# Optimization experiments

Measured on AMD Instinct MI355X. Metric: run time of the kernel, lower is better.

## Reference

```python
import jax, jax.numpy as jnp
import numpy as np

TEMP = 0.07
GAMMA1 = 0.8
GAMMA2 = 0.8
TAU = 0.1
BETA = 40.0
NUM_CT = 5
EPS = float(np.finfo(np.float32).eps)


def setup_inputs() -> dict:
    key = jax.random.key(0)
    ks = jax.random.split(key, 12)
    B, D, N, Bc = 8192, 512, 1000000, 4096
    img = jax.random.normal(ks[0], (B, D), jnp.float32)
    txt = jax.random.normal(ks[1], (B, D), jnp.float32)
    # CLIP-style unit-norm features keep sim in [-1,1] so exp() stays stable
    img = img / jnp.linalg.norm(img, axis=1, keepdims=True)
    txt = txt / jnp.linalg.norm(txt, axis=1, keepdims=True)
    image_ids = jax.random.randint(ks[2], (B,), 0, N)
    text_ids = jax.random.randint(ks[3], (B,), 0, N)
    slabel = jax.random.randint(ks[4], (B,), 0, 2)
    img_feas_c = jax.random.normal(ks[5], (Bc, D), jnp.float32)
    img_feas_c = img_feas_c / jnp.linalg.norm(img_feas_c, axis=1, keepdims=True)
    txt_feas_c = jax.random.normal(ks[6], (NUM_CT, D), jnp.float32)
    txt_feas_c = txt_feas_c / jnp.linalg.norm(txt_feas_c, axis=1, keepdims=True)
    labels_c = jax.random.randint(ks[7], (Bc,), 0, NUM_CT)
    last_loss_c = jax.random.uniform(ks[8], (Bc,), jnp.float32) * 2.0
    # persistent moving-average buffers (positive values, as they hold past exp-means)
    s_I = jax.random.uniform(ks[9], (N,), jnp.float32) + 0.5
    s_T = jax.random.uniform(ks[10], (N,), jnp.float32) + 0.5
    u = jnp.zeros((NUM_CT,), jnp.float32)
    return dict(image_features=img, text_features=txt, image_ids=image_ids,
                text_ids=text_ids, slabel=slabel, epoch=1,
                img_feas_c=img_feas_c, txt_feas_c=txt_feas_c, labels_c=labels_c,
                last_loss_c=last_loss_c, s_I=s_I, s_T=s_T, u=u)


def reference(image_features, text_features, image_ids, text_ids, slabel, epoch,
              img_feas_c, txt_feas_c, labels_c, last_loss_c, s_I, s_T, u):
    sg = jax.lax.stop_gradient
    # pairwise similarity GEMM  [B, B]
    sim = jnp.einsum('id,jd->ij', image_features, text_features)
    diag = jnp.diagonal(sim)
    pos = slabel == 1
    neg = ~pos
    pos_image_ids = image_ids[pos]
    pos_text_ids = text_ids[pos]
    # masked pairwise similarity differences: [P, B-P] and [B-P, P]
    image_diffs = (sim - diag[:, None])[pos][:, neg]
    text_diffs = (sim - diag[None, :])[neg][:, pos]
    image_diffs_d = sg(image_diffs / TEMP)
    text_diffs_d = sg(text_diffs / TEMP)
    exp_i = jnp.exp(image_diffs_d)
    exp_t = jnp.exp(text_diffs_d)
    g_I = jnp.mean(exp_i, axis=1, keepdims=True)   # [P, 1]
    g_T = jnp.mean(exp_t, axis=0, keepdims=True)   # [1, P]
    if epoch == 0:
        sI = g_I
        sT = g_T
    else:
        sI = ((1.0 - GAMMA1) * s_I[pos_image_ids] + GAMMA1 * g_I.squeeze()).reshape(g_I.shape)
        sT = ((1.0 - GAMMA1) * s_T[pos_text_ids] + GAMMA1 * g_T.squeeze()).reshape(g_T.shape)
    # persistent buffer scatter updates
    s_I_new = s_I.at[pos_image_ids].set(sI.squeeze())
    s_T_new = s_T.at[pos_text_ids].set(sT.squeeze())
    w_i = exp_i / (sI + EPS)
    w_t = exp_t / (sT + EPS)
    image_loss = jnp.mean(w_i * image_diffs, axis=1)
    text_loss = jnp.mean(w_t * text_diffs, axis=0)
    contrastive_loss = image_loss.mean() + text_loss.mean()
    # per-class CE penalty branch
    logits = (1.0 / TAU) * img_feas_c @ txt_feas_c.T           # [Bc, NUM_CT]
    logp = jax.nn.log_softmax(logits, axis=-1)
    ce = -logp[jnp.arange(logits.shape[0]), labels_c]          # [Bc]
    counts = jax.ops.segment_sum(jnp.ones_like(ce), labels_c, num_segments=NUM_CT)
    present = counts > 0
    safe_counts = jnp.maximum(counts, 1.0)
    mean_by_cls = jax.ops.segment_sum(ce, labels_c, num_segments=NUM_CT) / safe_counts
    mean_by_cls_last = jax.ops.segment_sum(last_loss_c, labels_c, num_segments=NUM_CT) / safe_counts
    cv = mean_by_cls - mean_by_cls_last
    u_sum = jnp.sum(jnp.where(present, u, 0.0))
    u_upd = jnp.where(u_sum == 0.0, sg(cv), (1.0 - GAMMA2) * u + GAMMA2 * sg(cv))
    u_new = jnp.where(present, u_upd, u)
    beta = BETA  # cosine=False
    cl = sg(jnp.maximum(beta * u_new, 0.0)) * mean_by_cls * TAU
    n_present = jnp.sum(present.astype(jnp.float32))
    constraint_mean = jnp.sum(jnp.where(present, cl, 0.0)) / n_present
    loss = contrastive_loss + constraint_mean
    return loss, s_I_new, s_T_new, u_new
```

## Files before the change

### kernel.cpp

```cpp
#include <hip/hip_runtime.h>

#define NBATCH 8192
#define DD 512
#define NIDS 1000000
#define BCNT 4096
#define NCT 5
#define INV_TEMP 14.285714285714286f
#define EPSF 1.1920929e-07f

typedef __attribute__((ext_vector_type(8))) short bf16x8;
typedef __attribute__((ext_vector_type(4))) float f32x4;
typedef __attribute__((ext_vector_type(8))) unsigned short u16x8;

#define OFF_LP     ((size_t)0)
#define OFF_CE1    ((size_t)1024)
#define OFF_CE2    ((size_t)2304)
#define OFF_CE3    ((size_t)3584)
#define OFF_POS    ((size_t)(32*1024))
#define OFF_RNK    ((size_t)(64*1024))
#define OFF_CNT    ((size_t)(96*1024))
#define OFF_DA     ((size_t)(100*1024))
#define OFF_RA0    ((size_t)(132*1024))
#define OFF_RB0    ((size_t)(164*1024))
#define OFF_RA1    ((size_t)(196*1024))
#define OFF_RB1    ((size_t)(228*1024))
#define OFF_SIV    ((size_t)(260*1024))
#define OFF_STV    ((size_t)(292*1024))
#define OFF_WINI   ((size_t)(324*1024))
#define OFF_WINT   (OFF_WINI + 4000000)
#define OFF_MA     (OFF_WINT + 4000000)
#define MATB       ((size_t)(8192*512*2))
#define OFF_MB     (OFF_MA + MATB)
#define OFF_MC     (OFF_MB + MATB)
#define OFF_MD     (OFF_MC + MATB)


__device__ __forceinline__ unsigned short f2bf(float x) {
    unsigned int u = __float_as_uint(x);
    unsigned int r = (u + 0x7fffu + ((u >> 16) & 1u)) >> 16;
    return (unsigned short)r;
}

__global__ __launch_bounds__(256) void k_pre(
        const float* __restrict__ sI, const float* __restrict__ sT,
        float* __restrict__ out,
        float* __restrict__ rA0, float* __restrict__ rB0,
        float* __restrict__ rA1, float* __restrict__ rB1,
        const int* __restrict__ slabel, int* __restrict__ pos,
        int* __restrict__ rnk, int* __restrict__ cnts,
        const float* __restrict__ imgc, const float* __restrict__ tfc,
        const int* __restrict__ labels, const float* __restrict__ lastl,
        float* __restrict__ ce1, float* __restrict__ ce2, float* __restrict__ ce3) {
    int bid = blockIdx.x;
    int tid = threadIdx.x;
    int iv = bid * 256 + tid;
    if (iv < NIDS) {
        out[1 + iv] = sI[iv];
        out[1 + NIDS + iv] = sT[iv];
    }
    if (iv < NBATCH) { rA0[iv] = 0.f; rB0[iv] = 0.f; rA1[iv] = 0.f; rB1[iv] = 0.f; }
    if (bid < 3907) return;

    if (bid == 3971) {
        __shared__ int sums[256];
        int base = tid * 32;
        int c = 0;
        for (int j = 0; j < 32; ++j) c += (slabel[base + j] == 1);
        sums[tid] = c;
        __syncthreads();
        for (int off = 1; off < 256; off <<= 1) {
            int add = (tid >= off) ? sums[tid - off] : 0;
            __syncthreads();
            sums[tid] += add;
            __syncthreads();
        }
        int p = sums[tid] - c;
        for (int j = 0; j < 32; ++j) {
            int idx = base + j;
            if (slabel[idx] == 1) { pos[p] = idx; rnk[idx] = p; p++; }
            else rnk[idx] = idx - p;
        }
        if (tid == 255) { cnts[0] = sums[255]; cnts[1] = NBATCH - sums[255]; }
    } else {
        int cb = bid - 3907;
        __shared__ float tS[NCT * DD];
        __shared__ float sce[NCT], scn[NCT], sls[NCT];
        for (int j = tid; j < NCT * DD; j += 256) tS[j] = tfc[j];
        if (tid < NCT) { sce[tid] = 0.f; scn[tid] = 0.f; sls[tid] = 0.f; }
        __syncthreads();
        int lane = tid & 63;
        int wid = tid >> 6;
        for (int it = 0; it < 16; ++it) {
            int r = it * 256 + cb * 4 + wid;
            const float4* ip = (const float4*)(imgc + (size_t)r * DD) + lane * 2;
            float4 a0 = ip[0], a1 = ip[1];
            float p[NCT];
#pragma unroll
            for (int c = 0; c < NCT; ++c) {
                const float* t = &tS[c * DD + lane * 8];
                p[c] = a0.x * t[0] + a0.y * t[1] + a0.z * t[2] + a0.w * t[3]
                     + a1.x * t[4] + a1.y * t[5] + a1.z * t[6] + a1.w * t[7];
            }
#pragma unroll
            for (int c = 0; c < NCT; ++c)
                for (int off = 32; off; off >>= 1) p[c] += __shfl_xor(p[c], off);
            if (lane == 0) {
                float l[NCT];
                float mx = -1e30f;
#pragma unroll
                for (int c = 0; c < NCT; ++c) { l[c] = p[c] * 10.0f; mx = fmaxf(mx, l[c]); }
                float ssum = 0.f;
#pragma unroll
                for (int c = 0; c < NCT; ++c) ssum += __expf(l[c] - mx);
                float lse = mx + __logf(ssum);
                int lb = labels[r];
                float ce = lse - l[lb];
                atomicAdd(&sce[lb], ce);
                atomicAdd(&scn[lb], 1.f);
                atomicAdd(&sls[lb], lastl[r]);
            }
        }
        __syncthreads();
        if (tid < NCT) {
            ce1[cb * 5 + tid] = sce[tid];
            ce2[cb * 5 + tid] = scn[tid];
            ce3[cb * 5 + tid] = sls[tid];
        }
    }
}

__global__ __launch_bounds__(256) void k_gather(
        const float* __restrict__ img, const float* __restrict__ txt,
        const int* __restrict__ slabel, const int* __restrict__ rnk,
        const int* __restrict__ image_ids, const int* __restrict__ text_ids,
        int* __restrict__ winI, int* __restrict__ winT,
        unsigned short* __restrict__ mA, unsigned short* __restrict__ mB,
        unsigned short* __restrict__ mC, unsigned short* __restrict__ mD,
        float* __restrict__ dA) {
    int tid = threadIdx.x;
    int kk = blockIdx.x * 256 + tid;
    if (kk < NBATCH) {
        winI[image_ids[kk]] = -1;
        winT[text_ids[kk]] = -1;
    }
    int i = blockIdx.x * 4 + (tid >> 6);
    int g = tid & 63;
    const float4* ip = (const float4*)(img + (size_t)i * DD) + g * 2;
    const float4* tp = (const float4*)(txt + (size_t)i * DD) + g * 2;
    float4 v0 = ip[0], v1 = ip[1], t0 = tp[0], t1 = tp[1];
    float part = v0.x * t0.x + v0.y * t0.y + v0.z * t0.z + v0.w * t0.w
               + v1.x * t1.x + v1.y * t1.y + v1.z * t1.z + v1.w * t1.w;
    for (int off = 32; off; off >>= 1) part += __shfl_xor(part, off);

    int lab = (slabel[i] == 1);
    int r = rnk[i];
    u16x8 oi, ot;
    oi[0] = f2bf(v0.x); oi[1] = f2bf(v0.y); oi[2] = f2bf(v0.z); oi[3] = f2bf(v0.w);
    oi[4] = f2bf(v1.x); oi[5] = f2bf(v1.y); oi[6] = f2bf(v1.z); oi[7] = f2bf(v1.w);
    ot[0] = f2bf(t0.x); ot[1] = f2bf(t0.y); ot[2] = f2bf(t0.z); ot[3] = f2bf(t0.w);
    ot[4] = f2bf(t1.x); ot[5] = f2bf(t1.y); ot[6] = f2bf(t1.z); ot[7] = f2bf(t1.w);

    int kc = g >> 2, gg = g & 3, rl = r & 127;
    int kb = (gg * 16) ^ ((rl & 6) << 3);
    size_t off = (size_t)(r >> 7) * 65536 + (size_t)kc * 4096 + rl * 32 + (kb >> 1);
    unsigned short* dI = lab ? mA : mD;
    unsigned short* dT = lab ? mC : mB;
    *(u16x8*)(dI + off) = oi;
    *(u16x8*)(dT + off) = ot;
    if (lab && g == 0) dA[r] = part;
}

__device__ __forceinline__ void gl16(const unsigned short* src, unsigned short* lds) {
    __builtin_amdgcn_global_load_lds((const __attribute__((address_space(1))) void*)src,
                                     (__attribute__((address_space(3))) void*)lds, 16, 0, 0);
}

#define VM4()  asm volatile("s_waitcnt vmcnt(4)" ::: "memory")
#define VM0()  asm volatile("s_waitcnt vmcnt(0)" ::: "memory")
#define BARR() asm volatile("s_barrier" ::: "memory")

__global__ __launch_bounds__(256) void k_gemm(
        const unsigned short* __restrict__ mA, const unsigned short* __restrict__ mB,
        const unsigned short* __restrict__ mC, const unsigned short* __restrict__ mD,
        const float* __restrict__ dA, const int* __restrict__ cnts,
        float* __restrict__ rA0, float* __restrict__ rB0,
        float* __restrict__ rA1, float* __restrict__ rB1) {
    int P = cnts[0], Nn = cnts[1];
    int bm = blockIdx.x * 128, bn = blockIdx.y * 128;
    if (bm >= P || bn >= Nn) return;
    int z = blockIdx.z;
    const unsigned short* Ap = (z ? mC : mA) + (size_t)blockIdx.x * 65536;
    const unsigned short* Bp = (z ? mD : mB) + (size_t)blockIdx.y * 65536;
    float* rA = z ? rA1 : rA0;
    float* rB = z ? rB1 : rB0;

    __shared__ __align__(16) char SRAW[36864];
    unsigned short* S0 = (unsigned short*)SRAW;

    int tid = threadIdx.x;
    int lane = tid & 63;
    int wid = tid >> 6;
    int wr = wid >> 1, wc = wid & 1;
    int soff = tid * 8;

    int kswz = ((lane >> 4) * 16) ^ ((lane & 6) << 3);
    int abyte = (wr * 64 + (lane & 15)) * 64 + kswz;
    int bbyte = (wc * 64 + (lane & 15)) * 64 + kswz;

    f32x4 acc[4][4];
#pragma unroll
    for (int m = 0; m < 4; ++m)
#pragma unroll
        for (int n = 0; n < 4; ++n) acc[m][n] = (f32x4){0.f, 0.f, 0.f, 0.f};

#define STAGE(kt, p) do { \
        gl16(Ap + (kt) * 4096 + soff,        S0 + (p) * 8192 + soff); \
        gl16(Ap + (kt) * 4096 + soff + 2048, S0 + (p) * 8192 + soff + 2048); \
        gl16(Bp + (kt) * 4096 + soff,        S0 + (p) * 8192 + 4096 + soff); \
        gl16(Bp + (kt) * 4096 + soff + 2048, S0 + (p) * 8192 + 4096 + soff + 2048); } while (0)

    STAGE(0, 0);
    STAGE(1, 1);
    VM4();
    BARR();

#pragma unroll
    for (int kt = 0; kt < 16; ++kt) {
        const int cur = kt & 1;
        bf16x8 af[4], bfv[4];
#pragma unroll
        for (int m = 0; m < 4; ++m)
            af[m] = *(const bf16x8*)((const char*)S0 + cur * 16384 + abyte + m * 1024);
#pragma unroll
        for (int n = 0; n < 4; ++n)
            bfv[n] = *(const bf16x8*)((const char*)S0 + cur * 16384 + 8192 + bbyte + n * 1024);
#pragma unroll
        for (int m = 0; m < 4; ++m)
#pragma unroll
            for (int n = 0; n < 4; ++n)
                acc[m][n] = __builtin_amdgcn_mfma_f32_16x16x32_bf16(af[m], bfv[n], acc[m][n], 0, 0, 0);
        if (kt < 15) {
            BARR();
            if (kt + 2 < 16) {
                STAGE(kt + 2, cur);
                VM4();
            } else {
                VM0();
            }
            BARR();
        }
    }
#undef STAGE

    BARR();
    float* F = (float*)SRAW;
    int col = lane & 15;
    int rsub = (lane >> 4) * 4;
    int rowbase = bm + wr * 64;
    int colb = bn + wc * 64 + col;
    int fb = ((wc << 7) + (wr << 6)) * 36 + col * 2;
#pragma unroll
    for (int m = 0; m < 4; ++m) {
#pragma unroll
        for (int r = 0; r < 4; ++r) {
            int wrow = m * 16 + rsub + r;
            float dv = dA[rowbase + wrow];
            float pa = 0.f, pb = 0.f;
#pragma unroll
            for (int n = 0; n < 4; ++n) {
                int gcol = colb + n * 16;
                float sv = acc[m][n][r];
                float df = sv - dv;
                float e = (gcol < Nn) ? __expf(df * INV_TEMP) : 0.f;
                pa += e;
                pb += e * df;
            }
            *(float2*)&F[fb + wrow * 36] = make_float2(pa, pb);
        }
    }
    BARR();
    {
        int row = tid >> 1;
        int half = tid & 1;
        const float4* Fr = (const float4*)&F[((half << 7) + row) * 36];
        float sa = 0.f, sb = 0.f;
#pragma unroll
        for (int q = 0; q < 8; ++q) {
            float4 v = Fr[q];
            sa += v.x + v.z;
            sb += v.y + v.w;
        }
        sa += __shfl_xor(sa, 1);
        sb += __shfl_xor(sb, 1);
        int grow = bm + row;
        if (!half && grow < P) {
            atomicAdd(&rA[grow], sa);
            atomicAdd(&rB[grow], sb);
        }
    }
}

__global__ void k_posfin(const int* __restrict__ cnts, const int* __restrict__ pos,
                         const float* __restrict__ rA0, const float* __restrict__ rB0,
                         const float* __restrict__ rA1, const float* __restrict__ rB1,
                         const int* __restrict__ image_ids, const int* __restrict__ text_ids,
                         const float* __restrict__ sIin, const float* __restrict__ sTin,
                         const int* __restrict__ epochp,
                         float* __restrict__ sIv, float* __restrict__ sTv,
                         int* __restrict__ winI, int* __restrict__ winT,
                         float* __restrict__ lp) {
    int k = blockIdx.x * 256 + threadIdx.x;
    int P = cnts[0], Nn = cnts[1];
    float invNn = 1.f / (float)Nn;
    int epoch = epochp[0];
    float lI = 0.f, lT = 0.f;
    if (k < P) {
        int i = pos[k];
        int idI = image_ids[i], idT = text_ids[i];
        float gI = rA0[k] * invNn;
        float sIvk = (epoch == 0) ? gI : 0.2f * sIin[idI] + 0.8f * gI;
        lI = (rB0[k] * invNn) / (sIvk + EPSF);
        float gT = rA1[k] * invNn;
        float sTvk = (epoch == 0) ? gT : 0.2f * sTin[idT] + 0.8f * gT;
        lT = (rB1[k] * invNn) / (sTvk + EPSF);
        sIv[k] = sIvk;
        sTv[k] = sTvk;
        atomicMax(&winI[idI], k);
        atomicMax(&winT[idT], k);
    }
    for (int off = 32; off; off >>= 1) { lI += __shfl_xor(lI, off); lT += __shfl_xor(lT, off); }
    if ((threadIdx.x & 63) == 0) {
        int slot = blockIdx.x * 4 + (threadIdx.x >> 6);
        lp[slot * 2] = lI;
        lp[slot * 2 + 1] = lT;
    }
}

__global__ void k_fin(const int* __restrict__ cnts, const int* __restrict__ pos,
                      const int* __restrict__ image_ids, const int* __restrict__ text_ids,
                      const int* __restrict__ winI, const int* __restrict__ winT,
                      const float* __restrict__ sIv, const float* __restrict__ sTv,
                      const float* __restrict__ lp, const float* __restrict__ ce1,
                      const float* __restrict__ ce2, const float* __restrict__ ce3,
                      const float* __restrict__ u, float* __restrict__ out) {
    int P = cnts[0];
    int k = blockIdx.x * 256 + threadIdx.x;
    if (k < P) {
        int i = pos[k];
        int a = image_ids[i];
        if (winI[a] == k) out[1 + a] = sIv[k];
        int b = text_ids[i];
        if (winT[b] == k) out[1 + NIDS + b] = sTv[k];
    }
    if (blockIdx.x == 0 && threadIdx.x < 64) {
        int lane = threadIdx.x;
        float lI = lp[2 * lane] + lp[2 * (lane + 64)];
        float lT = lp[2 * lane + 1] + lp[2 * (lane + 64) + 1];
        for (int off = 32; off; off >>= 1) { lI += __shfl_xor(lI, off); lT += __shfl_xor(lT, off); }
        float ce[NCT], cn[NCT], ls[NCT];
#pragma unroll
        for (int c = 0; c < NCT; ++c) {
            float a1 = ce1[lane * 5 + c], a2 = ce2[lane * 5 + c], a3 = ce3[lane * 5 + c];
            for (int off = 32; off; off >>= 1) {
                a1 += __shfl_xor(a1, off);
                a2 += __shfl_xor(a2, off);
                a3 += __shfl_xor(a3, off);
            }
            ce[c] = a1; cn[c] = a2; ls[c] = a3;
        }
        if (lane == 0) {
            float Pf = (float)P;
            float contrast = lI / Pf + lT / Pf;
            float u_sum = 0.f;
            float mc[NCT], cv[NCT], u_new[NCT];
            bool pres[NCT];
#pragma unroll
            for (int c = 0; c < NCT; ++c) {
                pres[c] = cn[c] > 0.f;
                float safe = fmaxf(cn[c], 1.f);
                mc[c] = ce[c] / safe;
                float ml = ls[c] / safe;
                cv[c] = mc[c] - ml;
                if (pres[c]) u_sum += u[c];
            }
            float np_ = 0.f, csum = 0.f;
#pragma unroll
            for (int c = 0; c < NCT; ++c) {
                float uu = (u_sum == 0.f) ? cv[c] : 0.2f * u[c] + 0.8f * cv[c];
                u_new[c] = pres[c] ? uu : u[c];
                if (pres[c]) {
                    np_ += 1.f;
                    csum += fmaxf(40.0f * u_new[c], 0.f) * mc[c] * 0.1f;
                }
                out[1 + 2 * NIDS + c] = u_new[c];
            }
            out[0] = contrast + csum / np_;
        }
    }
}

extern "C" void kernel_launch(void* const* d_in, const int* in_sizes, int n_in,
                              void* d_out, int out_size, void* d_ws, size_t ws_size,
                              hipStream_t stream) {
    const float* img = (const float*)d_in[0];
    const float* txt = (const float*)d_in[1];
    const int* image_ids = (const int*)d_in[2];
    const int* text_ids = (const int*)d_in[3];
    const int* slabel = (const int*)d_in[4];
    const int* epoch = (const int*)d_in[5];
    const float* imgc = (const float*)d_in[6];
    const float* tfc = (const float*)d_in[7];
    const int* labels = (const int*)d_in[8];
    const float* lastl = (const float*)d_in[9];
    const float* sI = (const float*)d_in[10];
    const float* sT = (const float*)d_in[11];
    const float* u = (const float*)d_in[12];
    float* out = (float*)d_out;
    char* ws = (char*)d_ws;

    float* lp = (float*)(ws + OFF_LP);
    float* ce1 = (float*)(ws + OFF_CE1);
    float* ce2 = (float*)(ws + OFF_CE2);
    float* ce3 = (float*)(ws + OFF_CE3);
    int* pos = (int*)(ws + OFF_POS);
    int* rnk = (int*)(ws + OFF_RNK);
    int* cnts = (int*)(ws + OFF_CNT);
    float* dA = (float*)(ws + OFF_DA);
    float* rA0 = (float*)(ws + OFF_RA0);
    float* rB0 = (float*)(ws + OFF_RB0);
    float* rA1 = (float*)(ws + OFF_RA1);
    float* rB1 = (float*)(ws + OFF_RB1);
    float* sIv = (float*)(ws + OFF_SIV);
    float* sTv = (float*)(ws + OFF_STV);
    int* winI = (int*)(ws + OFF_WINI);
    int* winT = (int*)(ws + OFF_WINT);
    unsigned short* mA = (unsigned short*)(ws + OFF_MA);
    unsigned short* mB = (unsigned short*)(ws + OFF_MB);
    unsigned short* mC = (unsigned short*)(ws + OFF_MC);
    unsigned short* mD = (unsigned short*)(ws + OFF_MD);

    k_pre<<<3972, 256, 0, stream>>>(sI, sT, out, rA0, rB0, rA1, rB1,
                                    slabel, pos, rnk, cnts,
                                    imgc, tfc, labels, lastl, ce1, ce2, ce3);
    k_gather<<<2048, 256, 0, stream>>>(img, txt, slabel, rnk, image_ids, text_ids,
                                       winI, winT, mA, mB, mC, mD, dA);
    k_gemm<<<dim3(64, 64, 2), 256, 0, stream>>>(mA, mB, mC, mD, dA, cnts, rA0, rB0, rA1, rB1);
    k_posfin<<<32, 256, 0, stream>>>(cnts, pos, rA0, rB0, rA1, rB1, image_ids, text_ids,
                                     sI, sT, epoch, sIv, sTv, winI, winT, lp);
    k_fin<<<32, 256, 0, stream>>>(cnts, pos, image_ids, text_ids, winI, winT,
                                  sIv, sTv, lp, ce1, ce2, ce3, u, out);
}
```

Baseline: 87.75 us.

## Switch similarity GEMM from bf16 to scaled fp8 MFMA

```diff
diff --git a/kernel.cpp b/kernel.cpp
--- a/kernel.cpp
+++ b/kernel.cpp
@@ -7,10 +7,11 @@
 #define NCT 5
 #define INV_TEMP 14.285714285714286f
 #define EPSF 1.1920929e-07f
-
-typedef __attribute__((ext_vector_type(8))) short bf16x8;
+#define FPSCALE 16.0f
+#define INV_SIMSCALE (1.0f / 256.0f)
+
 typedef __attribute__((ext_vector_type(4))) float f32x4;
-typedef __attribute__((ext_vector_type(8))) unsigned short u16x8;
+typedef __attribute__((ext_vector_type(2))) long lx2;
 
 #define OFF_LP     ((size_t)0)
 #define OFF_CE1    ((size_t)1024)
@@ -35,12 +36,6 @@
 #define OFF_MD     (OFF_MC + MATB)
 
 
-__device__ __forceinline__ unsigned short f2bf(float x) {
-    unsigned int u = __float_as_uint(x);
-    unsigned int r = (u + 0x7fffu + ((u >> 16) & 1u)) >> 16;
-    return (unsigned short)r;
-}
-
 __global__ __launch_bounds__(256) void k_pre(
         const float* __restrict__ sI, const float* __restrict__ sT,
         float* __restrict__ out,
@@ -134,8 +129,8 @@
         const int* __restrict__ slabel, const int* __restrict__ rnk,
         const int* __restrict__ image_ids, const int* __restrict__ text_ids,
         int* __restrict__ winI, int* __restrict__ winT,
-        unsigned short* __restrict__ mA, unsigned short* __restrict__ mB,
-        unsigned short* __restrict__ mC, unsigned short* __restrict__ mD,
+        unsigned char* __restrict__ mA, unsigned char* __restrict__ mB,
+        unsigned char* __restrict__ mC, unsigned char* __restrict__ mD,
         float* __restrict__ dA) {
     int tid = threadIdx.x;
     int kk = blockIdx.x * 256 + tid;
@@ -154,23 +149,29 @@
 
     int lab = (slabel[i] == 1);
     int r = rnk[i];
-    u16x8 oi, ot;
-    oi[0] = f2bf(v0.x); oi[1] = f2bf(v0.y); oi[2] = f2bf(v0.z); oi[3] = f2bf(v0.w);
-    oi[4] = f2bf(v1.x); oi[5] = f2bf(v1.y); oi[6] = f2bf(v1.z); oi[7] = f2bf(v1.w);
-    ot[0] = f2bf(t0.x); ot[1] = f2bf(t0.y); ot[2] = f2bf(t0.z); ot[3] = f2bf(t0.w);
-    ot[4] = f2bf(t1.x); ot[5] = f2bf(t1.y); ot[6] = f2bf(t1.z); ot[7] = f2bf(t1.w);
-
-    int kc = g >> 2, gg = g & 3, rl = r & 127;
-    int kb = (gg * 16) ^ ((rl & 6) << 3);
-    size_t off = (size_t)(r >> 7) * 65536 + (size_t)kc * 4096 + rl * 32 + (kb >> 1);
-    unsigned short* dI = lab ? mA : mD;
-    unsigned short* dT = lab ? mC : mB;
-    *(u16x8*)(dI + off) = oi;
-    *(u16x8*)(dT + off) = ot;
+
+    int ilo = __builtin_amdgcn_cvt_pk_fp8_f32(v0.x * FPSCALE, v0.y * FPSCALE, 0, 0);
+    ilo = __builtin_amdgcn_cvt_pk_fp8_f32(v0.z * FPSCALE, v0.w * FPSCALE, ilo, 1);
+    int ihi = __builtin_amdgcn_cvt_pk_fp8_f32(v1.x * FPSCALE, v1.y * FPSCALE, 0, 0);
+    ihi = __builtin_amdgcn_cvt_pk_fp8_f32(v1.z * FPSCALE, v1.w * FPSCALE, ihi, 1);
+    int tlo = __builtin_amdgcn_cvt_pk_fp8_f32(t0.x * FPSCALE, t0.y * FPSCALE, 0, 0);
+    tlo = __builtin_amdgcn_cvt_pk_fp8_f32(t0.z * FPSCALE, t0.w * FPSCALE, tlo, 1);
+    int thi = __builtin_amdgcn_cvt_pk_fp8_f32(t1.x * FPSCALE, t1.y * FPSCALE, 0, 0);
+    thi = __builtin_amdgcn_cvt_pk_fp8_f32(t1.z * FPSCALE, t1.w * FPSCALE, thi, 1);
+
+    int rl = r & 127;
+    int cp = g & 7;
+    int gran = cp & 3, half = cp >> 2;
+    int swb = ((gran * 16) ^ ((rl & 6) << 3)) + half * 8;
+    size_t off = (size_t)(r >> 7) * 65536 + (size_t)(g >> 3) * 8192 + rl * 64 + swb;
+    unsigned char* dI = lab ? mA : mD;
+    unsigned char* dT = lab ? mC : mB;
+    *(int2*)(dI + off) = make_int2(ilo, ihi);
+    *(int2*)(dT + off) = make_int2(tlo, thi);
     if (lab && g == 0) dA[r] = part;
 }
 
-__device__ __forceinline__ void gl16(const unsigned short* src, unsigned short* lds) {
+__device__ __forceinline__ void gl16(const void* src, void* lds) {
     __builtin_amdgcn_global_load_lds((const __attribute__((address_space(1))) void*)src,
                                      (__attribute__((address_space(3))) void*)lds, 16, 0, 0);
 }
@@ -180,8 +181,8 @@
 #define BARR() asm volatile("s_barrier" ::: "memory")
 
 __global__ __launch_bounds__(256) void k_gemm(
-        const unsigned short* __restrict__ mA, const unsigned short* __restrict__ mB,
-        const unsigned short* __restrict__ mC, const unsigned short* __restrict__ mD,
+        const unsigned char* __restrict__ mA, const unsigned char* __restrict__ mB,
+        const unsigned char* __restrict__ mC, const unsigned char* __restrict__ mD,
         const float* __restrict__ dA, const int* __restrict__ cnts,
         float* __restrict__ rA0, float* __restrict__ rB0,
         float* __restrict__ rA1, float* __restrict__ rB1) {
@@ -189,19 +190,19 @@
     int bm = blockIdx.x * 128, bn = blockIdx.y * 128;
     if (bm >= P || bn >= Nn) return;
     int z = blockIdx.z;
-    const unsigned short* Ap = (z ? mC : mA) + (size_t)blockIdx.x * 65536;
-    const unsigned short* Bp = (z ? mD : mB) + (size_t)blockIdx.y * 65536;
+    const unsigned char* Ap = (z ? mC : mA) + (size_t)blockIdx.x * 65536;
+    const unsigned char* Bp = (z ? mD : mB) + (size_t)blockIdx.y * 65536;
     float* rA = z ? rA1 : rA0;
     float* rB = z ? rB1 : rB0;
 
     __shared__ __align__(16) char SRAW[36864];
-    unsigned short* S0 = (unsigned short*)SRAW;
+    char* S = SRAW;
 
     int tid = threadIdx.x;
     int lane = tid & 63;
     int wid = tid >> 6;
     int wr = wid >> 1, wc = wid & 1;
-    int soff = tid * 8;
+    int bo = tid * 16;
 
     int kswz = ((lane >> 4) * 16) ^ ((lane & 6) << 3);
     int abyte = (wr * 64 + (lane & 15)) * 64 + kswz;
@@ -214,10 +215,10 @@
         for (int n = 0; n < 4; ++n) acc[m][n] = (f32x4){0.f, 0.f, 0.f, 0.f};
 
 #define STAGE(kt, p) do { \
-        gl16(Ap + (kt) * 4096 + soff,        S0 + (p) * 8192 + soff); \
-        gl16(Ap + (kt) * 4096 + soff + 2048, S0 + (p) * 8192 + soff + 2048); \
-        gl16(Bp + (kt) * 4096 + soff,        S0 + (p) * 8192 + 4096 + soff); \
-        gl16(Bp + (kt) * 4096 + soff + 2048, S0 + (p) * 8192 + 4096 + soff + 2048); } while (0)
+        gl16(Ap + (kt) * 8192 + bo,        S + (p) * 16384 + bo); \
+        gl16(Ap + (kt) * 8192 + bo + 4096, S + (p) * 16384 + bo + 4096); \
+        gl16(Bp + (kt) * 8192 + bo,        S + (p) * 16384 + 8192 + bo); \
+        gl16(Bp + (kt) * 8192 + bo + 4096, S + (p) * 16384 + 8192 + bo + 4096); } while (0)
 
     STAGE(0, 0);
     STAGE(1, 1);
@@ -225,23 +226,29 @@
     BARR();
 
 #pragma unroll
-    for (int kt = 0; kt < 16; ++kt) {
+    for (int kt = 0; kt < 8; ++kt) {
         const int cur = kt & 1;
-        bf16x8 af[4], bfv[4];
+        const char* base = S + cur * 16384;
+        lx2 af[4], bf[4];
 #pragma unroll
         for (int m = 0; m < 4; ++m)
-            af[m] = *(const bf16x8*)((const char*)S0 + cur * 16384 + abyte + m * 1024);
+            af[m] = *(const lx2*)(base + abyte + m * 1024);
 #pragma unroll
         for (int n = 0; n < 4; ++n)
-            bfv[n] = *(const bf16x8*)((const char*)S0 + cur * 16384 + 8192 + bbyte + n * 1024);
+            bf[n] = *(const lx2*)(base + 8192 + bbyte + n * 1024);
 #pragma unroll
         for (int m = 0; m < 4; ++m)
 #pragma unroll
             for (int n = 0; n < 4; ++n)
-                acc[m][n] = __builtin_amdgcn_mfma_f32_16x16x32_bf16(af[m], bfv[n], acc[m][n], 0, 0, 0);
-        if (kt < 15) {
+                acc[m][n] = __builtin_amdgcn_mfma_f32_16x16x32_fp8_fp8(af[m][0], bf[n][0], acc[m][n], 0, 0, 0);
+#pragma unroll
+        for (int m = 0; m < 4; ++m)
+#pragma unroll
+            for (int n = 0; n < 4; ++n)
+                acc[m][n] = __builtin_amdgcn_mfma_f32_16x16x32_fp8_fp8(af[m][1], bf[n][1], acc[m][n], 0, 0, 0);
+        if (kt < 7) {
             BARR();
-            if (kt + 2 < 16) {
+            if (kt + 2 < 8) {
                 STAGE(kt + 2, cur);
                 VM4();
             } else {
@@ -269,7 +276,7 @@
 #pragma unroll
             for (int n = 0; n < 4; ++n) {
                 int gcol = colb + n * 16;
-                float sv = acc[m][n][r];
+                float sv = acc[m][n][r] * INV_SIMSCALE;
                 float df = sv - dv;
                 float e = (gcol < Nn) ? __expf(df * INV_TEMP) : 0.f;
                 pa += e;
@@ -434,10 +441,10 @@
     float* sTv = (float*)(ws + OFF_STV);
     int* winI = (int*)(ws + OFF_WINI);
     int* winT = (int*)(ws + OFF_WINT);
-    unsigned short* mA = (unsigned short*)(ws + OFF_MA);
-    unsigned short* mB = (unsigned short*)(ws + OFF_MB);
-    unsigned short* mC = (unsigned short*)(ws + OFF_MC);
-    unsigned short* mD = (unsigned short*)(ws + OFF_MD);
+    unsigned char* mA = (unsigned char*)(ws + OFF_MA);
+    unsigned char* mB = (unsigned char*)(ws + OFF_MB);
+    unsigned char* mC = (unsigned char*)(ws + OFF_MC);
+    unsigned char* mD = (unsigned char*)(ws + OFF_MD);
 
     k_pre<<<3972, 256, 0, stream>>>(sI, sT, out, rA0, rB0, rA1, rB1,
                                     slabel, pos, rnk, cnts,
```

Measured after the change: 77.02 us. -12.2%, faster.
